# Kernel optimization log

Measured on AMD Instinct MI355X. Metric: run time of the kernel, lower is better.

The kernel has to match this reference:

```python
import jax, jax.numpy as jnp
import numpy as np

N = 100000      # nodes
E = 800000      # directed edges per branch
HID = 128
FOUT = 128
HEADS = 2
LAYERS = 3      # convlayer
JK_LAYERS = 3
H2 = (JK_LAYERS * HID) // 2   # PyG JK-LSTM hidden size = 192
N_AA = 26
N_SS = 3


def setup_inputs() -> dict:
    key = jax.random.key(0)
    ks = iter(jax.random.split(key, 32))
    def nrm(shape, scale=0.05):
        return jax.random.normal(next(ks), shape, dtype=jnp.float32) * scale
    return {
        "x_idx": jax.random.randint(next(ks), (N, 2), 0, N_SS),
        "x_flt": jax.random.normal(next(ks), (N, 5), dtype=jnp.float32),
        "edge_index_l": jax.random.randint(next(ks), (2, E), 0, N),
        "edge_index_r": jax.random.randint(next(ks), (2, E), 0, N),
        "emb_aa": nrm((2, N_AA, HID - 5)),          # [branch, vocab, hid-5]
        "emb_ss": nrm((2, N_SS, HID - 5)),
        "conv_W": nrm((2, LAYERS, HID, HEADS * HID)),
        "conv_att_src": nrm((2, LAYERS, HEADS, HID)),
        "conv_att_dst": nrm((2, LAYERS, HEADS, HID)),
        "conv_bias": nrm((2, LAYERS, HID)),
        "lstm_Wih": nrm((2, 2, 4 * H2, HID)),        # [branch, direction, 4H2, hid]
        "lstm_Whh": nrm((2, 2, 4 * H2, H2)),
        "lstm_bih": nrm((2, 2, 4 * H2)),
        "lstm_bhh": nrm((2, 2, 4 * H2)),
        "jk_att_W": nrm((2, 2 * H2)),
        "jk_att_b": nrm((2,)),
        "dummy_W": nrm((2, HID, HID)),
        "dummy_b": nrm((2, HID)),
        "fin_W": nrm((4, HID, FOUT)),
        "fin_b": nrm((4, FOUT)),
        "last_W": nrm((FOUT,)),                      # Linear(fout,1,bias=False)
    }


def _gat_conv(x, src, dst, W, att_src, att_dst, bias):
    # PyG GATConv, concat=False (mean over heads), leaky_relu slope 0.2
    n = x.shape[0]
    h, c = att_src.shape
    xh = (x @ W).reshape(n, h, c)                         # [N,H,C]
    a_src = jnp.einsum('nhc,hc->nh', xh, att_src)
    a_dst = jnp.einsum('nhc,hc->nh', xh, att_dst)
    e = jax.nn.leaky_relu(a_src[src] + a_dst[dst], 0.2)   # [E,H]
    m = jax.ops.segment_max(e, dst, num_segments=n)
    ex = jnp.exp(e - m[dst])
    denom = jax.ops.segment_sum(ex, dst, num_segments=n)
    alpha = ex / (denom[dst] + 1e-16)                     # segment softmax over dst
    out = jax.ops.segment_sum(xh[src] * alpha[:, :, None], dst, num_segments=n)
    return out.mean(axis=1) + bias                        # [N,C]


def _lstm_dir(xs, Wih, Whh, bih, bhh, reverse):
    # xs: [L,N,C]; single-layer LSTM, torch gate order i,f,g,o
    n = xs.shape[1]
    h2 = Whh.shape[1]
    b = bih + bhh
    def cell(carry, xt):
        h, c = carry
        g = xt @ Wih.T + h @ Whh.T + b
        i, f, gg, o = jnp.split(g, 4, axis=-1)
        c = jax.nn.sigmoid(f) * c + jax.nn.sigmoid(i) * jnp.tanh(gg)
        h = jax.nn.sigmoid(o) * jnp.tanh(c)
        return (h, c), h
    init = (jnp.zeros((n, h2), xs.dtype), jnp.zeros((n, h2), xs.dtype))
    _, hs = jax.lax.scan(cell, init, xs, reverse=reverse)
    return hs  # [L,N,H2]


def _jk(xs, Wih, Whh, bih, bhh, att_w, att_b):
    # PyG JumpingKnowledge('lstm'): bi-LSTM over layer axis + scalar attention
    hf = _lstm_dir(xs, Wih[0], Whh[0], bih[0], bhh[0], False)
    hb = _lstm_dir(xs, Wih[1], Whh[1], bih[1], bhh[1], True)
    h = jnp.concatenate([hf, hb], axis=-1)                # [L,N,2H2]
    a = jax.nn.softmax(jnp.einsum('lnh,h->ln', h, att_w) + att_b, axis=0)
    return (xs * a[..., None]).sum(axis=0)                # [N,C]


def _forward(x_idx, x_flt, edge_index_l, edge_index_r, emb_aa, emb_ss,
             conv_W, conv_att_src, conv_att_dst, conv_bias,
             lstm_Wih, lstm_Whh, lstm_bih, lstm_bhh, jk_att_W, jk_att_b,
             dummy_W, dummy_b, fin_W, fin_b, last_W):
    n = x_idx.shape[0]
    loops = jnp.arange(n)  # GATConv add_self_loops=True
    src_l = jnp.concatenate([edge_index_l[0], loops]); dst_l = jnp.concatenate([edge_index_l[1], loops])
    src_r = jnp.concatenate([edge_index_r[0], loops]); dst_r = jnp.concatenate([edge_index_r[1], loops])
    x_l = jnp.concatenate([emb_aa[0][x_idx[:, 0]] + emb_ss[0][x_idx[:, 1]], x_flt], axis=1)
    x_r = jnp.concatenate([emb_aa[1][x_idx[:, 0]] + emb_ss[1][x_idx[:, 1]], x_flt], axis=1)
    xs_l, xs_r = [], []
    for i in range(LAYERS):
        mean = (x_l + x_r) * 0.5
        o_l = mean + jax.nn.relu(_gat_conv(x_l, src_l, dst_l, conv_W[0, i], conv_att_src[0, i], conv_att_dst[0, i], conv_bias[0, i]))
        o_r = mean + jax.nn.relu(_gat_conv(x_r, src_r, dst_r, conv_W[1, i], conv_att_src[1, i], conv_att_dst[1, i], conv_bias[1, i]))
        x_l, x_r = o_l, o_r
        xs_l.append(x_l); xs_r.append(x_r)
    jk_l = _jk(jnp.stack(xs_l), lstm_Wih[0], lstm_Whh[0], lstm_bih[0], lstm_bhh[0], jk_att_W[0], jk_att_b[0])
    jk_r = _jk(jnp.stack(xs_r), lstm_Wih[1], lstm_Whh[1], lstm_bih[1], lstm_bhh[1], jk_att_W[1], jk_att_b[1])
    sq_l = jk_l @ dummy_W[0] + dummy_b[0]
    sq_r = jk_r @ dummy_W[1] + dummy_b[1]
    feats = [jk_l, sq_l, jk_r, sq_r]
    outs = [feats[i] @ fin_W[i] + fin_b[i] for i in range(4)]
    alpha = jax.nn.softmax(jnp.stack([o @ last_W for o in outs], axis=1), axis=1)  # [N,4]
    nodeemb = sum(outs[i] * alpha[:, i:i + 1] for i in range(4))
    return nodeemb


def reference(x_idx, x_flt, edge_index_l, edge_index_r, emb_aa, emb_ss,
              conv_W, conv_att_src, conv_att_dst, conv_bias,
              lstm_Wih, lstm_Whh, lstm_bih, lstm_bhh, jk_att_W, jk_att_b,
              dummy_W, dummy_b, fin_W, fin_b, last_W):
    return _forward(x_idx, x_flt, edge_index_l, edge_index_r, emb_aa, emb_ss,
                    conv_W, conv_att_src, conv_att_dst, conv_bias,
                    lstm_Wih, lstm_Whh, lstm_bih, lstm_bhh, jk_att_W, jk_att_b,
                    dummy_W, dummy_b, fin_W, fin_b, last_W)
```

## Files before the change

kernel.cpp:

```cpp
#include <hip/hip_runtime.h>
#include <cstddef>
#include <cstdint>

#define N_NODES 100000
#define N_EDGES 800000
#define EL_TOT  900000
#define HID 128
#define H2  192
#define G4  768
#define CH3 50000
#define BK  32
#define LDST 32

typedef unsigned short bf16;
typedef __attribute__((ext_vector_type(8))) short bf16x8v;
typedef __attribute__((ext_vector_type(4))) float f32x4v;

#define AS1 __attribute__((address_space(1)))
#define AS3 __attribute__((address_space(3)))

__device__ __forceinline__ void async16(const bf16* g, bf16* l) {
    __builtin_amdgcn_global_load_lds((AS1 void*)g, (AS3 void*)l, 16, 0, 0);
}


__device__ __forceinline__ float b2f(bf16 u) {
    return __uint_as_float(((unsigned)u) << 16);
// ... 12 lines not shown
}

__device__ __forceinline__ float x0_val(int c, int ia, int is_, int n,
                                        const float* __restrict__ embA,
                                        const float* __restrict__ embS,
                                        const float* __restrict__ xflt) {
    return (c < 123) ? (embA[ia * 123 + c] + embS[is_ * 123 + c])
                     : xflt[n * 5 + (c - 123)];
}

__device__ __forceinline__ int lstm_perm(int j) {
    int w = j & 63, tt = j >> 6;
    return (w >> 4) * 192 + tt * 16 + (w & 15);
}

__device__ __forceinline__ bool swz_tile(int R, int ntile, int& bm0, int& bn0) {
    const int id = blockIdx.x;
    const int xcd = id & 7;
    const int s = id >> 3;
    const int nt = s % ntile;
    const int yp = (s / ntile) * 8 + xcd;
    if (yp * 128 >= R) return false;
    bm0 = yp * 128; bn0 = nt * 128;
    return true;
}
static inline int swz_grid(int R, int ntile) {
    int panels = (R + 127) / 128;
    return 8 * ntile * ((panels + 7) / 8);
}


__global__ void sentinel_kernel(float* out, int n, float val) {
    int t = blockIdx.x * blockDim.x + threadIdx.x;
    if (t < n) out[t] = val;
}

__global__ void bsum_perm_kernel(const float* __restrict__ bih,
                                 const float* __restrict__ bhh,
// ... 25 lines not shown
    int per = K * M;
    int bt = (int)(t / per);
    int rem = (int)(t % per);
    int m = rem / K, k = rem % K;
    out[t] = f2b(in[(size_t)bt * per + (size_t)k * M + m]);
}


__global__ void deg_kernel(const int* __restrict__ dst, int* __restrict__ deg) {
    int t = blockIdx.x * blockDim.x + threadIdx.x;
    if (t >= EL_TOT) return;
    int d = (t < N_EDGES) ? dst[t] : (t - N_EDGES);
    atomicAdd(&deg[d], 1);
}

__global__ void scan_kernel(const int* __restrict__ deg, int* __restrict__ offs, int n) {
    __shared__ int sdata[1024];
    __shared__ int carry;
    if (threadIdx.x == 0) carry = 0;
    __syncthreads();
    for (int base = 0; base < n; base += 1024) {
        int i = base + (int)threadIdx.x;
        int v = (i < n) ? deg[i] : 0;
        sdata[threadIdx.x] = v;
        __syncthreads();
        for (int off = 1; off < 1024; off <<= 1) {
            int t = (threadIdx.x >= (unsigned)off) ? sdata[threadIdx.x - off] : 0;
            __syncthreads();
            sdata[threadIdx.x] += t;
            __syncthreads();
        }
        if (i < n) offs[i + 1] = carry + sdata[threadIdx.x];
        __syncthreads();
        if (threadIdx.x == 1023) carry += sdata[1023];
        __syncthreads();
    }
    if (threadIdx.x == 0) offs[0] = 0;
}

__global__ void copy_int_kernel(const int* __restrict__ a, int* __restrict__ b, int n) {
    int t = blockIdx.x * blockDim.x + threadIdx.x;
    if (t < n) b[t] = a[t];
}

__global__ void fill_kernel(const int* __restrict__ srcrow,
                            const int* __restrict__ dstrow,
                            int* __restrict__ pos, int* __restrict__ srcs) {
    int t = blockIdx.x * blockDim.x + threadIdx.x;
    if (t >= EL_TOT) return;
    int s, d;
    if (t < N_EDGES) { s = srcrow[t]; d = dstrow[t]; }
    else             { s = d = t - N_EDGES; }
    int p = atomicAdd(&pos[d], 1);
    srcs[p] = s;
}

template<typename TC>
__global__ __launch_bounds__(256) void mfma_gemm_kernel(
    const bf16* __restrict__ A1, const bf16* __restrict__ B1, int K1,
    const bf16* __restrict__ A2, const bf16* __restrict__ B2, int K2,
    TC* __restrict__ C, const float* __restrict__ bias, int R, int M) {
    __shared__ bf16 As[2][128 * LDST];
    __shared__ bf16 Bs[2][128 * LDST];
    int bm0, bn0;
    if (!swz_tile(R, M >> 7, bm0, bn0)) return;
    const int tid = threadIdx.x;
    const int lane = tid & 63;
    const int wave = tid >> 6;
    const int wm = (wave & 1) * 64, wn = (wave >> 1) * 64;
    const int l15 = lane & 15;
    const int q8 = (lane >> 4) * 8;
    const int lr = lane >> 2;
    const int lc = (lane & 3) * 8;

    f32x4v acc[4][4];
#pragma unroll
    for (int i = 0; i < 4; ++i)
#pragma unroll
        for (int j = 0; j < 4; ++j) acc[i][j] = (f32x4v)(0.0f);

    const int n1 = K1 / BK;
    const int n2 = A2 ? (K2 / BK) : 0;
    const int ns = n1 + n2;

    auto stage = [&](int buf, int s) {
        const bf16* Ap; const bf16* Bp; int K, k0;
        if (s < n1) { Ap = A1; Bp = B1; K = K1; k0 = s * BK; }
        else        { Ap = A2; Bp = B2; K = K2; k0 = (s - n1) * BK; }
#pragma unroll
        for (int rnd = 0; rnd < 2; ++rnd) {
            const int rbase = wave * 16 + rnd * 64;
            const int row = rbase + lr;
            int ga = bm0 + row; ga = (ga < R) ? ga : (R - 1);
            async16(Ap + (size_t)ga * K + k0 + lc, &As[buf][rbase * LDST]);
            async16(Bp + (size_t)(bn0 + row) * K + k0 + lc, &Bs[buf][rbase * LDST]);
        }
    };

    stage(0, 0);
    __syncthreads();
    for (int s = 0; s < ns; ++s) {
        const int cur = s & 1;
        if (s + 1 < ns) stage(cur ^ 1, s + 1);
        bf16x8v af[4], bfv[4];
#pragma unroll
        for (int i = 0; i < 4; ++i) {
            af[i]  = *(const bf16x8v*)&As[cur][(wm + i * 16 + l15) * LDST + q8];
            bfv[i] = *(const bf16x8v*)&Bs[cur][(wn + i * 16 + l15) * LDST + q8];
        }
#pragma unroll
        for (int i = 0; i < 4; ++i)
#pragma unroll
            for (int j = 0; j < 4; ++j)
                acc[i][j] = __builtin_amdgcn_mfma_f32_16x16x32_bf16(
                    af[i], bfv[j], acc[i][j], 0, 0, 0);
        __syncthreads();
    }

#pragma unroll
    for (int i = 0; i < 4; ++i) {
        const int row0 = bm0 + wm + i * 16 + (lane >> 4) * 4;
#pragma unroll
        for (int j = 0; j < 4; ++j) {
            const int col = bn0 + wn + j * 16 + l15;
            const float bv = bias ? bias[col] : 0.f;
#pragma unroll
            for (int r = 0; r < 4; ++r) {
                const int gr = row0 + r;
                if (gr < R) stE(C, (size_t)gr * M + col, acc[i][j][r] + bv);
            }
        }
    }
}

template<typename TC>
static void mfma_gemm(const bf16* A1, const bf16* B1, int K1,
                      const bf16* A2, const bf16* B2, int K2,
                      TC* C, const float* bias, int R, int M, hipStream_t s) {
    mfma_gemm_kernel<TC><<<swz_grid(R, M / 128), 256, 0, s>>>(
        A1, B1, K1, A2, B2, K2, C, bias, R, M);
}

__global__ __launch_bounds__(256) void lstm_gemm4_kernel(
    const bf16* __restrict__ hist, const bf16* __restrict__ Wib,
    const bf16* __restrict__ Whb, const float* __restrict__ bsum,
    const float* __restrict__ jkw, float* __restrict__ scores,
    bf16* __restrict__ cbase, const bf16* __restrict__ hin,
    bf16* __restrict__ hout, long long hcstride, int st, int combo0, int R) {
    __shared__ bf16 As[2][128 * LDST];
    __shared__ bf16 Bs[2][128 * LDST];
    int bm0, bn0;
    if (!swz_tile(R, G4 >> 7, bm0, bn0)) return;

    const int combo = combo0 + (int)blockIdx.y;
    const int b = combo >> 1, dir = combo & 1;
    const int l = dir ? (2 - st) : st;
    const bool first = (st == 0);
    const bf16* A1 = hist + (size_t)(b * 3 + l) * R * HID;
    const bf16* B1 = Wib + (size_t)combo * G4 * HID;
    const bf16* A2 = hin + (size_t)combo * hcstride;
    const bf16* B2 = Whb + (size_t)combo * G4 * H2;
    const float* bias = bsum + (size_t)combo * G4;
    const float* aw = jkw + (size_t)b * 2 * H2 + (size_t)dir * H2;
    float* score = scores + (size_t)(b * 3 + l) * R;
    bf16* c_state = cbase + (size_t)combo * hcstride;
    bf16* h_o = hout + (size_t)combo * hcstride;

    const int tid = threadIdx.x;
    const int lane = tid & 63;
    const int wave = tid >> 6;
    const int wm = (wave & 1) * 64, wn = (wave >> 1) * 64;
    const int l15 = lane & 15;
    const int q = lane >> 4;
    const int q8 = q * 8;
    const int lr = lane >> 2;
    const int lc = (lane & 3) * 8;

    f32x4v acc[4][4];
#pragma unroll
    for (int i = 0; i < 4; ++i)
#pragma unroll
        for (int j = 0; j < 4; ++j) acc[i][j] = (f32x4v)(0.0f);

    const int n1 = HID / BK;
    const int n2 = first ? 0 : (H2 / BK);
    const int ns = n1 + n2;

    auto stage = [&](int buf, int s) {
        const bf16* Ap; const bf16* Bp; int K, k0;
        if (s < n1) { Ap = A1; Bp = B1; K = HID; k0 = s * BK; }
        else        { Ap = A2; Bp = B2; K = H2;  k0 = (s - n1) * BK; }
#pragma unroll
        for (int rnd = 0; rnd < 2; ++rnd) {
            const int rbase = wave * 16 + rnd * 64;
            const int row = rbase + lr;
            int ga = bm0 + row; ga = (ga < R) ? ga : (R - 1);
            async16(Ap + (size_t)ga * K + k0 + lc, &As[buf][rbase * LDST]);
            async16(Bp + (size_t)(bn0 + row) * K + k0 + lc, &Bs[buf][rbase * LDST]);
        }
    };

    stage(0, 0);
    __syncthreads();
    for (int s = 0; s < ns; ++s) {
        const int cur = s & 1;
        if (s + 1 < ns) stage(cur ^ 1, s + 1);
        bf16x8v af[4], bfv[4];
#pragma unroll
        for (int i = 0; i < 4; ++i) {
            af[i]  = *(const bf16x8v*)&As[cur][(wm + i * 16 + l15) * LDST + q8];
            bfv[i] = *(const bf16x8v*)&Bs[cur][(wn + i * 16 + l15) * LDST + q8];
        }
#pragma unroll
        for (int i = 0; i < 4; ++i)
#pragma unroll
            for (int j = 0; j < 4; ++j)
                acc[i][j] = __builtin_amdgcn_mfma_f32_16x16x32_bf16(
                    af[i], bfv[j], acc[i][j], 0, 0, 0);
        __syncthreads();
    }

    const int u = ((bn0 + wn) >> 6) * 16 + l15;
    const float awu = aw[u];
    float bv[4];
#pragma unroll
    for (int j = 0; j < 4; ++j) bv[j] = bias[bn0 + wn + j * 16 + l15];
    float psum[4][4];
#pragma unroll
    for (int i = 0; i < 4; ++i) {
        const int row0 = bm0 + wm + i * 16 + q * 4;
#pragma unroll
        for (int r = 0; r < 4; ++r) {
            const int gr = row0 + r;
            const bool ok = gr < R;
            float ig = acc[i][0][r] + bv[0];
            float fg = acc[i][1][r] + bv[1];
            float gg = acc[i][2][r] + bv[2];
            float og = acc[i][3][r] + bv[3];
            float si = 1.f / (1.f + __expf(-ig));
            float sf = 1.f / (1.f + __expf(-fg));
            float so = 1.f / (1.f + __expf(-og));
            float co = (ok && !first) ? b2f(c_state[(size_t)gr * H2 + u]) : 0.f;
            float cn = sf * co + si * ftanh(gg);
            float hn = so * ftanh(cn);
            if (ok) {
                c_state[(size_t)gr * H2 + u] = f2b(cn);
                h_o[(size_t)gr * H2 + u] = f2b(hn);
            }
            psum[i][r] = hn * awu;
        }
    }
#pragma unroll
    for (int m = 1; m < 16; m <<= 1)
#pragma unroll
        for (int i = 0; i < 4; ++i)
#pragma unroll
            for (int r = 0; r < 4; ++r)
                psum[i][r] += __shfl_xor(psum[i][r], m);
    if (l15 == 0) {
#pragma unroll
        for (int i = 0; i < 4; ++i)
#pragma unroll
            for (int r = 0; r < 4; ++r) {
                const int gr = bm0 + wm + i * 16 + q * 4 + r;
                if (gr < R) atomicAdd(&score[gr], psum[i][r]);
            }
    }
}

__global__ __launch_bounds__(256) void mfma_gemm_x0_kernel(
    const int* __restrict__ xidx, const float* __restrict__ xflt,
    const float* __restrict__ embA, const float* __restrict__ embS,
    const bf16* __restrict__ B1, bf16* __restrict__ C, int R, int M) {
    __shared__ bf16 As[128 * LDST];
    __shared__ bf16 Bs[128 * LDST];
    int bm0, bn0;
    if (!swz_tile(R, M >> 7, bm0, bn0)) return;
    const int tid = threadIdx.x;
    const int lane = tid & 63;
    const int wave = tid >> 6;
    const int wm = (wave & 1) * 64, wn = (wave >> 1) * 64;
    const int l15 = lane & 15;
    const int q8 = (lane >> 4) * 8;
    const int srow = tid >> 2;
    const int scol = (tid & 3) * 8;
    const int lr = lane >> 2;
    const int lc = (lane & 3) * 8;

    f32x4v acc[4][4];
#pragma unroll
    for (int i = 0; i < 4; ++i)
#pragma unroll
        for (int j = 0; j < 4; ++j) acc[i][j] = (f32x4v)(0.0f);

    for (int k0 = 0; k0 < 128; k0 += BK) {
#pragma unroll
        for (int rnd = 0; rnd < 2; ++rnd) {
            {
                int row = srow + rnd * 64;
                int ga = bm0 + row; ga = (ga < R) ? ga : (R - 1);
                int ia = xidx[2 * ga], is_ = xidx[2 * ga + 1];
                bf16 tmp[8];
#pragma unroll
                for (int t = 0; t < 8; ++t)
                    tmp[t] = f2b(x0_val(k0 + scol + t, ia, is_, ga, embA, embS, xflt));
                *(int4*)&As[row * LDST + scol] = *(const int4*)tmp;
            }
            {
                const int rbase = wave * 16 + rnd * 64;
                int row = rbase + lr;
                async16(B1 + (size_t)(bn0 + row) * 128 + k0 + lc, &Bs[rbase * LDST]);
            }
        }
        __syncthreads();
        bf16x8v af[4], bfv[4];
#pragma unroll
        for (int i = 0; i < 4; ++i) {
            af[i]  = *(const bf16x8v*)&As[(wm + i * 16 + l15) * LDST + q8];
            bfv[i] = *(const bf16x8v*)&Bs[(wn + i * 16 + l15) * LDST + q8];
        }
#pragma unroll
        for (int i = 0; i < 4; ++i)
#pragma unroll
            for (int j = 0; j < 4; ++j)
                acc[i][j] = __builtin_amdgcn_mfma_f32_16x16x32_bf16(
                    af[i], bfv[j], acc[i][j], 0, 0, 0);
        __syncthreads();
    }
#pragma unroll
    for (int i = 0; i < 4; ++i) {
        const int row0 = bm0 + wm + i * 16 + (lane >> 4) * 4;
#pragma unroll
        for (int j = 0; j < 4; ++j) {
            const int col = bn0 + wn + j * 16 + l15;
#pragma unroll
            for (int r = 0; r < 4; ++r) {
                const int gr = row0 + r;
                if (gr < R) C[(size_t)gr * M + col] = f2b(acc[i][j][r]);
            }
        }
    }
}


__global__ __launch_bounds__(256) void att_kernel(
    const bf16* __restrict__ xh, const float* __restrict__ as_,
    const float* __restrict__ ad_, float* __restrict__ asrc, float* __restrict__ adst) {
    int w = (blockIdx.x * blockDim.x + threadIdx.x) >> 6;
    int lane = threadIdx.x & 63;
    if (w >= N_NODES) return;
    const bf16* row = xh + (size_t)w * 256;
    float x0 = b2f(row[lane]), x1 = b2f(row[64 + lane]);
    float x2 = b2f(row[128 + lane]), x3 = b2f(row[192 + lane]);
// ... 16 lines not shown
__global__ __launch_bounds__(256) void agg_kernel(
    const bf16* __restrict__ xh, const float* __restrict__ asrc,
    const float* __restrict__ adst, const int* __restrict__ offs,
    const int* __restrict__ srcs,
    const bf16* __restrict__ xprev_l, const bf16* __restrict__ xprev_r,
    const int* __restrict__ xidx, const float* __restrict__ xflt,
    const float* __restrict__ embAl, const float* __restrict__ embSl,
    const float* __restrict__ embAr, const float* __restrict__ embSr,
    const float* __restrict__ bias, bf16* __restrict__ outx) {
    int n = (blockIdx.x * blockDim.x + threadIdx.x) >> 6;
    int lane = threadIdx.x & 63;
    if (n >= N_NODES) return;
    const int start = offs[n], end = offs[n + 1];
    const float ad0 = adst[2 * n], ad1 = adst[2 * n + 1];

    float m0 = -1e30f, m1 = -1e30f;
    for (int j = start + lane; j < end; j += 64) {
        int s = srcs[j];
        float2 a2 = *(const float2*)(asrc + 2 * s);
        m0 = fmaxf(m0, lrelu02(a2.x + ad0));
        m1 = fmaxf(m1, lrelu02(a2.y + ad1));
    }
    for (int o = 1; o < 64; o <<= 1) {
        m0 = fmaxf(m0, __shfl_xor(m0, o));
        m1 = fmaxf(m1, __shfl_xor(m1, o));
    }

    const int eh = lane >> 5;
    const int l32 = lane & 31;
    const int head = l32 >> 4;
    const int l15 = l32 & 15;
    const int col = head * 128 + l15 * 8;
    const float mh = head ? m1 : m0;
    const float adh = head ? ad1 : ad0;

    float acc[8] = {0.f, 0.f, 0.f, 0.f, 0.f, 0.f, 0.f, 0.f};
    float dsum = 0.f;
#pragma unroll 2
    for (int j = start; j < end; j += 2) {
        int e = j + eh;
        if (e < end) {
            int s = srcs[e];
            float a = asrc[2 * s + head] + adh;
            float al = __expf(lrelu02(a) - mh);
            if (l15 == 0) dsum += al;
            int4 v = *(const int4*)(xh + (size_t)s * 256 + col);
            const int* w = (const int*)&v;
#pragma unroll
            for (int t = 0; t < 4; ++t) {
                float lo = __uint_as_float(((unsigned)w[t]) << 16);
                float hi = __uint_as_float(((unsigned)w[t]) & 0xffff0000u);
                acc[2 * t]     += lo * al;
                acc[2 * t + 1] += hi * al;
            }
        }
    }
#pragma unroll
    for (int t = 0; t < 8; ++t) acc[t] += __shfl_xor(acc[t], 32);
    dsum += __shfl_xor(dsum, 32);
// ... 114 lines not shown
    const float* jkw     = (const float*)d_in[14];
    const float* dummy_W = (const float*)d_in[16];
    const float* dummy_b = (const float*)d_in[17];
    const float* fin_W   = (const float*)d_in[18];
    const float* fin_b   = (const float*)d_in[19];
    const float* last_W  = (const float*)d_in[20];
    float* out = (float*)d_out;

    const long long S = (long long)N_NODES * HID;
    char* ws = (char*)d_ws;
    long long off = 0;

    bf16* hist = (bf16*)(ws + off);  off += align1k(6 * S * 2);
    float* scores = (float*)(ws + off); off += align1k(6LL * N_NODES * 4);
    float* bsum   = (float*)(ws + off); off += align1k(4LL * G4 * 4);
    bf16* Wih_b   = (bf16*)(ws + off); off += align1k(4LL * G4 * HID * 2);
    bf16* Whh_b   = (bf16*)(ws + off); off += align1k(4LL * G4 * H2 * 2);
    bf16* dummyWt = (bf16*)(ws + off); off += align1k(2LL * 128 * 128 * 2);
    bf16* finWt   = (bf16*)(ws + off); off += align1k(4LL * 128 * 128 * 2);

    char* BIG = ws + off;
    const long long slot0 = align1k(2 * S * 2);
    const long long slot1 = align1k((long long)N_NODES * H2 * 2);
    const long long hcsz  = align1k(4LL * N_NODES * H2 * 2);
    const long long needC = off + slot0 + slot1;
    const long long needA = off + 3 * hcsz;

    if ((long long)ws_size < needC) {
        float val = 200000.0f + (float)(ws_size >> 20);
        sentinel_kernel<<<(N_NODES * HID + 255) / 256, 256, 0, stream>>>(
            out, N_NODES * HID, val);
        return;
    }
    const bool tierA = (long long)ws_size >= needA;

    bf16* xh  = (bf16*)BIG;
    bf16* jkb = (bf16*)BIG;
    int* ibase = (int*)(BIG + slot0);
    int *deg[2], *offs[2], *pos[2], *srcs[2];
    long long io = 0;
    for (int b = 0; b < 2; ++b) {
        deg[b]  = ibase + io; io += N_NODES;
        offs[b] = ibase + io; io += N_NODES + 1;
        pos[b]  = ibase + io; io += N_NODES;
        srcs[b] = ibase + io; io += EL_TOT;
    }
    long long io4a = ((io * 4 + 15) & ~15LL);
    float* asrc = (float*)(BIG + slot0 + io4a);
    float* adst = asrc + 2LL * N_NODES;
    bf16* convWt = (bf16*)(BIG + slot0 + io4a + 4LL * N_NODES * 4);
    bf16* cC = (bf16*)(BIG + slot0);
    bf16* hC = (bf16*)BIG;
    bf16* c4  = (bf16*)BIG;
    bf16* hp0 = (bf16*)(BIG + hcsz);
    bf16* hp1 = (bf16*)(BIG + 2 * hcsz);

    const float* embA[2] = {emb_aa, emb_aa + 26 * 123};
    const float* embS[2] = {emb_ss, emb_ss + 3 * 123};

    bsum_perm_kernel<<<12, 256, 0, stream>>>(bih, bhh, bsum);
    trans_kernel<<<(6 * 128 * 256 + 255) / 256, 256, 0, stream>>>(
        conv_W, convWt, 6, 128, 256);
    lstm_w_perm_kernel<<<(4 * G4 * HID + 255) / 256, 256, 0, stream>>>(
        Wih, Wih_b, HID);
    lstm_w_perm_kernel<<<(4 * G4 * H2 + 255) / 256, 256, 0, stream>>>(
        Whh, Whh_b, H2);
    trans_kernel<<<(2 * 128 * 128 + 255) / 256, 256, 0, stream>>>(
        dummy_W, dummyWt, 2, 128, 128);
    trans_kernel<<<(4 * 128 * 128 + 255) / 256, 256, 0, stream>>>(
        fin_W, finWt, 4, 128, 128);
    for (int b = 0; b < 2; ++b) {
        const int* ei = b ? ei_r : ei_l;
        hipMemsetAsync(deg[b], 0, N_NODES * sizeof(int), stream);
        deg_kernel<<<(EL_TOT + 255) / 256, 256, 0, stream>>>(ei + N_EDGES, deg[b]);
        scan_kernel<<<1, 1024, 0, stream>>>(deg[b], offs[b], N_NODES);
        copy_int_kernel<<<(N_NODES + 255) / 256, 256, 0, stream>>>(offs[b], pos[b], N_NODES);
        fill_kernel<<<(EL_TOT + 255) / 256, 256, 0, stream>>>(
            ei, ei + N_EDGES, pos[b], srcs[b]);
    }

    for (int i = 0; i < 3; ++i) {
        for (int b = 0; b < 2; ++b) {
            const bf16* Wc = convWt + (size_t)(b * 3 + i) * 256 * 128;
            if (i == 0) {
                mfma_gemm_x0_kernel<<<swz_grid(N_NODES, 2), 256, 0, stream>>>(
                    x_idx, x_flt, embA[b], embS[b], Wc, xh, N_NODES, 256);
            } else {
                mfma_gemm<bf16>(hist + (size_t)(b * 3 + i - 1) * S, Wc, 128,
                                nullptr, nullptr, 0, xh, nullptr, N_NODES, 256, stream);
            }
            att_kernel<<<25000, 256, 0, stream>>>(
                xh, att_s + (size_t)(b * 3 + i) * 2 * HID,
                att_d + (size_t)(b * 3 + i) * 2 * HID, asrc, adst);
            const bf16* xpl = (i == 0) ? nullptr : hist + (size_t)(i - 1) * S;
            const bf16* xpr = (i == 0) ? nullptr : hist + (size_t)(3 + i - 1) * S;
            agg_kernel<<<25000, 256, 0, stream>>>(
                xh, asrc, adst, offs[b], srcs[b], xpl, xpr,
                (i == 0) ? x_idx : nullptr, x_flt,
                embA[0], embS[0], embA[1], embS[1],
                conv_b + (size_t)(b * 3 + i) * HID, hist + (size_t)(b * 3 + i) * S);
        }
    }

    hipMemsetAsync(scores, 0, (size_t)6 * N_NODES * 4, stream);
    const int gx = swz_grid(N_NODES, 6);
    if (tierA) {
        for (int st = 0; st < 3; ++st) {
            const bf16* hin = (st & 1) ? hp0 : hp1;
            bf16* hout = (st & 1) ? hp1 : hp0;
            lstm_gemm4_kernel<<<dim3(gx, 4), 256, 0, stream>>>(
                hist, Wih_b, Whh_b, bsum, jkw, scores, c4, hin, hout,
                (long long)N_NODES * H2, st, 0, N_NODES);
        }
    } else {
        for (int b = 0; b < 2; ++b)
            for (int dir = 0; dir < 2; ++dir)
                for (int st = 0; st < 3; ++st)
                    lstm_gemm4_kernel<<<dim3(gx, 1), 256, 0, stream>>>(
                        hist, Wih_b, Whh_b, bsum, jkw, scores, cC, hC, hC,
                        0LL, st, b * 2 + dir, N_NODES);
    }
    for (int b = 0; b < 2; ++b)
        jkfin_kernel<<<25000, 256, 0, stream>>>(
            scores + (size_t)b * 3 * N_NODES,
            hist + (size_t)b * 3 * S, hist + (size_t)(b * 3 + 1) * S,
            hist + (size_t)(b * 3 + 2) * S, jkb + (size_t)b * S);

    float* f3 = (float*)hist;
    bf16* jkl = jkb; bf16* jkr = jkb + S;
    for (long long c3 = 0; c3 < N_NODES; c3 += CH3) {
        int Rr = (int)((N_NODES - c3) < CH3 ? (N_NODES - c3) : CH3);
        float* o0 = f3;
        float* o1 = f3 + 1LL * CH3 * HID;
        float* o2 = f3 + 2LL * CH3 * HID;
        float* o3 = f3 + 3LL * CH3 * HID;
        bf16* sql = (bf16*)(f3 + 4LL * CH3 * HID);
        bf16* sqr = sql + (long long)CH3 * HID;
        mfma_gemm<bf16>(jkl + c3 * HID, dummyWt, 128, nullptr, nullptr, 0,
                        sql, dummy_b, Rr, 128, stream);
        mfma_gemm<bf16>(jkr + c3 * HID, dummyWt + 16384, 128, nullptr, nullptr, 0,
                        sqr, dummy_b + 128, Rr, 128, stream);
        mfma_gemm<float>(jkl + c3 * HID, finWt, 128, nullptr, nullptr, 0,
                         o0, fin_b, Rr, 128, stream);
        mfma_gemm<float>(sql, finWt + 16384, 128, nullptr, nullptr, 0,
                         o1, fin_b + 128, Rr, 128, stream);
        mfma_gemm<float>(jkr + c3 * HID, finWt + 2 * 16384, 128, nullptr, nullptr, 0,
                         o2, fin_b + 256, Rr, 128, stream);
        mfma_gemm<float>(sqr, finWt + 3 * 16384, 128, nullptr, nullptr, 0,
                         o3, fin_b + 384, Rr, 128, stream);
        final_kernel<<<(Rr + 3) / 4, 256, 0, stream>>>(
            o0, o1, o2, o3, last_W, out, Rr, c3);
    }
}
```

Baseline: 3.453 ms.

## Parallelize CSR scan, widen GEMM tiles, batch final GEMMs, drop softmax max pass

The single-block degree scan becomes a three-phase multi-block scan that covers both branches and writes the fill positions directly, which removes the copy kernel. The GEMM and LSTM kernels now compute 256-column tiles so each A tile is loaded once per row panel. The final dummy/fin GEMMs are batched into launches indexed by grid y. The LSTM path is simplified to a single per-combo schedule that uses the output buffer as h scratch. The aggregation kernel drops its segment-max pass and exponentiates raw attention logits, which saves a pass over the edges but risks overflow for large logits.

```diff
diff --git a/kernel.cpp b/kernel.cpp
--- a/kernel.cpp
+++ b/kernel.cpp
@@ -11,6 +11,7 @@
 #define CH3 50000
 #define BK  32
 #define LDST 32
+#define SCANB 98
 
 typedef unsigned short bf16;
 typedef __attribute__((ext_vector_type(8))) short bf16x8v;
@@ -53,14 +54,14 @@
     return (w >> 4) * 192 + tt * 16 + (w & 15);
 }
 
-__device__ __forceinline__ bool swz_tile(int R, int ntile, int& bm0, int& bn0) {
+__device__ __forceinline__ bool swz_tile(int R, int ntile, int& bm0, int& nt) {
     const int id = blockIdx.x;
     const int xcd = id & 7;
     const int s = id >> 3;
-    const int nt = s % ntile;
+    nt = s % ntile;
     const int yp = (s / ntile) * 8 + xcd;
     if (yp * 128 >= R) return false;
-    bm0 = yp * 128; bn0 = nt * 128;
+    bm0 = yp * 128;
     return true;
 }
 static inline int swz_grid(int R, int ntile) {
@@ -116,33 +117,57 @@
     atomicAdd(&deg[d], 1);
 }
 
-__global__ void scan_kernel(const int* __restrict__ deg, int* __restrict__ offs, int n) {
+__global__ void scan1_kernel(const int* __restrict__ deg0, const int* __restrict__ deg1,
+                             int* __restrict__ tmp0, int* __restrict__ tmp1,
+                             int* __restrict__ bsums) {
     __shared__ int sdata[1024];
-    __shared__ int carry;
-    if (threadIdx.x == 0) carry = 0;
+    const int b = blockIdx.y;
+    const int* deg = b ? deg1 : deg0;
+    int* tmp = b ? tmp1 : tmp0;
+    int i = blockIdx.x * 1024 + threadIdx.x;
+    int v = (i < N_NODES) ? deg[i] : 0;
+    sdata[threadIdx.x] = v;
     __syncthreads();
-    for (int base = 0; base < n; base += 1024) {
-        int i = base + (int)threadIdx.x;
-        int v = (i < n) ? deg[i] : 0;
-        sdata[threadIdx.x] = v;
+    for (int off = 1; off < 1024; off <<= 1) {
+        int t = (threadIdx.x >= (unsigned)off) ? sdata[threadIdx.x - off] : 0;
         __syncthreads();
-        for (int off = 1; off < 1024; off <<= 1) {
-            int t = (threadIdx.x >= (unsigned)off) ? sdata[threadIdx.x - off] : 0;
-            __syncthreads();
-            sdata[threadIdx.x] += t;
-            __syncthreads();
-        }
-        if (i < n) offs[i + 1] = carry + sdata[threadIdx.x];
+        sdata[threadIdx.x] += t;
         __syncthreads();
-        if (threadIdx.x == 1023) carry += sdata[1023];
-        __syncthreads();
-    }
-    if (threadIdx.x == 0) offs[0] = 0;
-}
-
-__global__ void copy_int_kernel(const int* __restrict__ a, int* __restrict__ b, int n) {
-    int t = blockIdx.x * blockDim.x + threadIdx.x;
-    if (t < n) b[t] = a[t];
+    }
+    if (i < N_NODES) tmp[i] = sdata[threadIdx.x];
+    if (threadIdx.x == 1023) bsums[b * SCANB + blockIdx.x] = sdata[1023];
+}
+
+__global__ void scan2_kernel(int* __restrict__ bsums) {
+    int b = threadIdx.x;
+    if (b < 2) {
+        int c = 0;
+        for (int k = 0; k < SCANB; ++k) {
+            int t = bsums[b * SCANB + k];
+            bsums[b * SCANB + k] = c;
+            c += t;
+        }
+    }
+}
+
+__global__ void scan3_kernel(const int* __restrict__ bsums,
+                             const int* __restrict__ deg0, const int* __restrict__ deg1,
+                             const int* __restrict__ tmp0, const int* __restrict__ tmp1,
+                             int* __restrict__ offs0, int* __restrict__ offs1,
+                             int* __restrict__ pos0, int* __restrict__ pos1) {
+    const int b = blockIdx.y;
+    const int* deg = b ? deg1 : deg0;
+    const int* tmp = b ? tmp1 : tmp0;
+    int* offs = b ? offs1 : offs0;
+    int* pos = b ? pos1 : pos0;
+    int carry = bsums[b * SCANB + blockIdx.x];
+    int i = blockIdx.x * 1024 + threadIdx.x;
+    if (i < N_NODES) {
+        int inc = tmp[i] + carry;
+        offs[i + 1] = inc;
+        pos[i] = inc - deg[i];
+    }
+    if (i == 0) offs[0] = 0;
 }
 
 __global__ void fill_kernel(const int* __restrict__ srcrow,
@@ -157,15 +182,13 @@
     srcs[p] = s;
 }
 
-template<typename TC>
-__global__ __launch_bounds__(256) void mfma_gemm_kernel(
+template<typename TC, int NT>
+__device__ __forceinline__ void gemm_body(
     const bf16* __restrict__ A1, const bf16* __restrict__ B1, int K1,
-    const bf16* __restrict__ A2, const bf16* __restrict__ B2, int K2,
-    TC* __restrict__ C, const float* __restrict__ bias, int R, int M) {
+    TC* __restrict__ C, const float* __restrict__ bias, int R, int M,
+    int bm0, int bn0) {
     __shared__ bf16 As[2][128 * LDST];
-    __shared__ bf16 Bs[2][128 * LDST];
-    int bm0, bn0;
-    if (!swz_tile(R, M >> 7, bm0, bn0)) return;
+    __shared__ bf16 Bs[2][128 * NT * LDST];
     const int tid = threadIdx.x;
     const int lane = tid & 63;
     const int wave = tid >> 6;
@@ -175,27 +198,26 @@
     const int lr = lane >> 2;
     const int lc = (lane & 3) * 8;
 
-    f32x4v acc[4][4];
+    f32x4v acc[4][4 * NT];
 #pragma unroll
     for (int i = 0; i < 4; ++i)
 #pragma unroll
-        for (int j = 0; j < 4; ++j) acc[i][j] = (f32x4v)(0.0f);
-
-    const int n1 = K1 / BK;
-    const int n2 = A2 ? (K2 / BK) : 0;
-    const int ns = n1 + n2;
-
+        for (int j = 0; j < 4 * NT; ++j) acc[i][j] = (f32x4v)(0.0f);
+
+    const int ns = K1 / BK;
     auto stage = [&](int buf, int s) {
-        const bf16* Ap; const bf16* Bp; int K, k0;
-        if (s < n1) { Ap = A1; Bp = B1; K = K1; k0 = s * BK; }
-        else        { Ap = A2; Bp = B2; K = K2; k0 = (s - n1) * BK; }
+        const int k0 = s * BK;
 #pragma unroll
         for (int rnd = 0; rnd < 2; ++rnd) {
             const int rbase = wave * 16 + rnd * 64;
-            const int row = rbase + lr;
-            int ga = bm0 + row; ga = (ga < R) ? ga : (R - 1);
-            async16(Ap + (size_t)ga * K + k0 + lc, &As[buf][rbase * LDST]);
-            async16(Bp + (size_t)(bn0 + row) * K + k0 + lc, &Bs[buf][rbase * LDST]);
+            int ga = bm0 + rbase + lr; ga = (ga < R) ? ga : (R - 1);
+            async16(A1 + (size_t)ga * K1 + k0 + lc, &As[buf][rbase * LDST]);
+        }
+#pragma unroll
+        for (int rnd = 0; rnd < 2 * NT; ++rnd) {
+            const int rbase = wave * 16 + rnd * 64;
+            async16(B1 + (size_t)(bn0 + rbase + lr) * K1 + k0 + lc,
+                    &Bs[buf][rbase * LDST]);
         }
     };
 
@@ -204,16 +226,18 @@
     for (int s = 0; s < ns; ++s) {
         const int cur = s & 1;
         if (s + 1 < ns) stage(cur ^ 1, s + 1);
-        bf16x8v af[4], bfv[4];
-#pragma unroll
-        for (int i = 0; i < 4; ++i) {
-            af[i]  = *(const bf16x8v*)&As[cur][(wm + i * 16 + l15) * LDST + q8];
-            bfv[i] = *(const bf16x8v*)&Bs[cur][(wn + i * 16 + l15) * LDST + q8];
-        }
+        bf16x8v af[4], bfv[4 * NT];
 #pragma unroll
         for (int i = 0; i < 4; ++i)
-#pragma unroll
-            for (int j = 0; j < 4; ++j)
+            af[i] = *(const bf16x8v*)&As[cur][(wm + i * 16 + l15) * LDST + q8];
+#pragma unroll
+        for (int j = 0; j < 4 * NT; ++j)
+            bfv[j] = *(const bf16x8v*)
+                &Bs[cur][((j >> 2) * 128 + wn + (j & 3) * 16 + l15) * LDST + q8];
+#pragma unroll
+        for (int i = 0; i < 4; ++i)
+#pragma unroll
+            for (int j = 0; j < 4 * NT; ++j)
                 acc[i][j] = __builtin_amdgcn_mfma_f32_16x16x32_bf16(
                     af[i], bfv[j], acc[i][j], 0, 0, 0);
         __syncthreads();
@@ -223,8 +247,8 @@
     for (int i = 0; i < 4; ++i) {
         const int row0 = bm0 + wm + i * 16 + (lane >> 4) * 4;
 #pragma unroll
-        for (int j = 0; j < 4; ++j) {
-            const int col = bn0 + wn + j * 16 + l15;
+        for (int j = 0; j < 4 * NT; ++j) {
+            const int col = bn0 + (j >> 2) * 128 + wn + (j & 3) * 16 + l15;
             const float bv = bias ? bias[col] : 0.f;
 #pragma unroll
             for (int r = 0; r < 4; ++r) {
@@ -235,39 +259,41 @@
     }
 }
 
+template<typename TC, int NT>
+__global__ __launch_bounds__(256) void mfma_gemm_kernel(
+    const bf16* __restrict__ A1, const bf16* __restrict__ B1, int K1,
+    TC* __restrict__ C, const float* __restrict__ bias, int R, int M) {
+    int bm0, nt;
+    if (!swz_tile(R, M / (128 * NT), bm0, nt)) return;
+    gemm_body<TC, NT>(A1, B1, K1, C, bias, R, M, bm0, nt * 128 * NT);
+}
+
 template<typename TC>
-static void mfma_gemm(const bf16* A1, const bf16* B1, int K1,
-                      const bf16* A2, const bf16* B2, int K2,
-                      TC* C, const float* bias, int R, int M, hipStream_t s) {
-    mfma_gemm_kernel<TC><<<swz_grid(R, M / 128), 256, 0, s>>>(
-        A1, B1, K1, A2, B2, K2, C, bias, R, M);
-}
-
-__global__ __launch_bounds__(256) void lstm_gemm4_kernel(
-    const bf16* __restrict__ hist, const bf16* __restrict__ Wib,
-    const bf16* __restrict__ Whb, const float* __restrict__ bsum,
-    const float* __restrict__ jkw, float* __restrict__ scores,
-    bf16* __restrict__ cbase, const bf16* __restrict__ hin,
-    bf16* __restrict__ hout, long long hcstride, int st, int combo0, int R) {
+__global__ __launch_bounds__(256) void mfma_gemm_b_kernel(
+    const bf16* a0, const bf16* a1, const bf16* a2, const bf16* a3,
+    const bf16* __restrict__ Bbase,
+    TC* c0, TC* c1, TC* c2, TC* c3,
+    const float* __restrict__ bias, int R) {
+    int bm0, nt;
+    if (!swz_tile(R, 1, bm0, nt)) return;
+    const int y = blockIdx.y;
+    const bf16* A1 = (y == 0) ? a0 : (y == 1) ? a1 : (y == 2) ? a2 : a3;
+    TC* C = (y == 0) ? c0 : (y == 1) ? c1 : (y == 2) ? c2 : c3;
+    gemm_body<TC, 1>(A1, Bbase + (size_t)y * 128 * 128, 128, C,
+                     bias + (size_t)y * 128, R, 128, bm0, 0);
+}
+
+__global__ __launch_bounds__(256) void lstm_gemm_kernel(
+    const bf16* __restrict__ A1, const bf16* __restrict__ B1,
+    const bf16* __restrict__ A2, const bf16* __restrict__ B2,
+    const float* __restrict__ bias, bf16* __restrict__ c_state,
+    bf16* __restrict__ h_out, const float* __restrict__ aw,
+    float* __restrict__ score, int R) {
     __shared__ bf16 As[2][128 * LDST];
-    __shared__ bf16 Bs[2][128 * LDST];
-    int bm0, bn0;
-    if (!swz_tile(R, G4 >> 7, bm0, bn0)) return;
-
-    const int combo = combo0 + (int)blockIdx.y;
-    const int b = combo >> 1, dir = combo & 1;
-    const int l = dir ? (2 - st) : st;
-    const bool first = (st == 0);
-    const bf16* A1 = hist + (size_t)(b * 3 + l) * R * HID;
-    const bf16* B1 = Wib + (size_t)combo * G4 * HID;
-    const bf16* A2 = hin + (size_t)combo * hcstride;
-    const bf16* B2 = Whb + (size_t)combo * G4 * H2;
-    const float* bias = bsum + (size_t)combo * G4;
-    const float* aw = jkw + (size_t)b * 2 * H2 + (size_t)dir * H2;
-    float* score = scores + (size_t)(b * 3 + l) * R;
-    bf16* c_state = cbase + (size_t)combo * hcstride;
-    bf16* h_o = hout + (size_t)combo * hcstride;
-
+    __shared__ bf16 Bs[2][256 * LDST];
+    int bm0, nt;
+    if (!swz_tile(R, 3, bm0, nt)) return;
+    const int bn0 = nt * 256;
     const int tid = threadIdx.x;
     const int lane = tid & 63;
     const int wave = tid >> 6;
@@ -277,16 +303,16 @@
     const int q8 = q * 8;
     const int lr = lane >> 2;
     const int lc = (lane & 3) * 8;
-
-    f32x4v acc[4][4];
+    const bool first = (A2 == nullptr);
+
+    f32x4v acc[4][8];
 #pragma unroll
     for (int i = 0; i < 4; ++i)
 #pragma unroll
-        for (int j = 0; j < 4; ++j) acc[i][j] = (f32x4v)(0.0f);
+        for (int j = 0; j < 8; ++j) acc[i][j] = (f32x4v)(0.0f);
 
     const int n1 = HID / BK;
-    const int n2 = first ? 0 : (H2 / BK);
-    const int ns = n1 + n2;
+    const int ns = n1 + (first ? 0 : (H2 / BK));
 
     auto stage = [&](int buf, int s) {
         const bf16* Ap; const bf16* Bp; int K, k0;
@@ -295,10 +321,14 @@
 #pragma unroll
         for (int rnd = 0; rnd < 2; ++rnd) {
             const int rbase = wave * 16 + rnd * 64;
-            const int row = rbase + lr;
-            int ga = bm0 + row; ga = (ga < R) ? ga : (R - 1);
+            int ga = bm0 + rbase + lr; ga = (ga < R) ? ga : (R - 1);
             async16(Ap + (size_t)ga * K + k0 + lc, &As[buf][rbase * LDST]);
-            async16(Bp + (size_t)(bn0 + row) * K + k0 + lc, &Bs[buf][rbase * LDST]);
+        }
+#pragma unroll
+        for (int rnd = 0; rnd < 4; ++rnd) {
+            const int rbase = wave * 16 + rnd * 64;
+            async16(Bp + (size_t)(bn0 + rbase + lr) * K + k0 + lc,
+                    &Bs[buf][rbase * LDST]);
         }
     };
 
@@ -307,26 +337,30 @@
     for (int s = 0; s < ns; ++s) {
         const int cur = s & 1;
         if (s + 1 < ns) stage(cur ^ 1, s + 1);
-        bf16x8v af[4], bfv[4];
-#pragma unroll
-        for (int i = 0; i < 4; ++i) {
-            af[i]  = *(const bf16x8v*)&As[cur][(wm + i * 16 + l15) * LDST + q8];
-            bfv[i] = *(const bf16x8v*)&Bs[cur][(wn + i * 16 + l15) * LDST + q8];
-        }
+        bf16x8v af[4], bfv[8];
 #pragma unroll
         for (int i = 0; i < 4; ++i)
-#pragma unroll
-            for (int j = 0; j < 4; ++j)
+            af[i] = *(const bf16x8v*)&As[cur][(wm + i * 16 + l15) * LDST + q8];
+#pragma unroll
+        for (int j = 0; j < 8; ++j)
+            bfv[j] = *(const bf16x8v*)
+                &Bs[cur][((j >> 2) * 128 + wn + (j & 3) * 16 + l15) * LDST + q8];
+#pragma unroll
+        for (int i = 0; i < 4; ++i)
+#pragma unroll
+            for (int j = 0; j < 8; ++j)
                 acc[i][j] = __builtin_amdgcn_mfma_f32_16x16x32_bf16(
                     af[i], bfv[j], acc[i][j], 0, 0, 0);
         __syncthreads();
     }
 
-    const int u = ((bn0 + wn) >> 6) * 16 + l15;
-    const float awu = aw[u];
-    float bv[4];
-#pragma unroll
-    for (int j = 0; j < 4; ++j) bv[j] = bias[bn0 + wn + j * 16 + l15];
+    const int u0 = ((bn0 + wn) >> 6) * 16 + l15;
+    const int u1 = ((bn0 + 128 + wn) >> 6) * 16 + l15;
+    const float aw0 = aw[u0], aw1 = aw[u1];
+    float bv[8];
+#pragma unroll
+    for (int j = 0; j < 8; ++j)
+        bv[j] = bias[bn0 + (j >> 2) * 128 + wn + (j & 3) * 16 + l15];
     float psum[4][4];
 #pragma unroll
     for (int i = 0; i < 4; ++i) {
@@ -335,21 +369,26 @@
         for (int r = 0; r < 4; ++r) {
             const int gr = row0 + r;
             const bool ok = gr < R;
-            float ig = acc[i][0][r] + bv[0];
-            float fg = acc[i][1][r] + bv[1];
-            float gg = acc[i][2][r] + bv[2];
-            float og = acc[i][3][r] + bv[3];
-            float si = 1.f / (1.f + __expf(-ig));
-            float sf = 1.f / (1.f + __expf(-fg));
-            float so = 1.f / (1.f + __expf(-og));
-            float co = (ok && !first) ? b2f(c_state[(size_t)gr * H2 + u]) : 0.f;
-            float cn = sf * co + si * ftanh(gg);
-            float hn = so * ftanh(cn);
-            if (ok) {
-                c_state[(size_t)gr * H2 + u] = f2b(cn);
-                h_o[(size_t)gr * H2 + u] = f2b(hn);
+            float hn[2];
+#pragma unroll
+            for (int jj = 0; jj < 2; ++jj) {
+                const int u = jj ? u1 : u0;
+                float ig = acc[i][jj * 4 + 0][r] + bv[jj * 4 + 0];
+                float fg = acc[i][jj * 4 + 1][r] + bv[jj * 4 + 1];
+                float gg = acc[i][jj * 4 + 2][r] + bv[jj * 4 + 2];
+                float og = acc[i][jj * 4 + 3][r] + bv[jj * 4 + 3];
+                float si = 1.f / (1.f + __expf(-ig));
+                float sf = 1.f / (1.f + __expf(-fg));
+                float so = 1.f / (1.f + __expf(-og));
+                float co = (ok && !first) ? b2f(c_state[(size_t)gr * H2 + u]) : 0.f;
+                float cn = sf * co + si * ftanh(gg);
+                hn[jj] = so * ftanh(cn);
+                if (ok) {
+                    c_state[(size_t)gr * H2 + u] = f2b(cn);
+                    h_out[(size_t)gr * H2 + u] = f2b(hn[jj]);
+                }
             }
-            psum[i][r] = hn * awu;
+            psum[i][r] = hn[0] * aw0 + hn[1] * aw1;
         }
     }
 #pragma unroll
@@ -373,11 +412,11 @@
 __global__ __launch_bounds__(256) void mfma_gemm_x0_kernel(
     const int* __restrict__ xidx, const float* __restrict__ xflt,
     const float* __restrict__ embA, const float* __restrict__ embS,
-    const bf16* __restrict__ B1, bf16* __restrict__ C, int R, int M) {
+    const bf16* __restrict__ B1, bf16* __restrict__ C, int R) {
     __shared__ bf16 As[128 * LDST];
-    __shared__ bf16 Bs[128 * LDST];
-    int bm0, bn0;
-    if (!swz_tile(R, M >> 7, bm0, bn0)) return;
+    __shared__ bf16 Bs[256 * LDST];
+    int bm0, nt;
+    if (!swz_tile(R, 1, bm0, nt)) return;
     const int tid = threadIdx.x;
     const int lane = tid & 63;
     const int wave = tid >> 6;
@@ -389,42 +428,42 @@
     const int lr = lane >> 2;
     const int lc = (lane & 3) * 8;
 
-    f32x4v acc[4][4];
+    f32x4v acc[4][8];
 #pragma unroll
     for (int i = 0; i < 4; ++i)
 #pragma unroll
-        for (int j = 0; j < 4; ++j) acc[i][j] = (f32x4v)(0.0f);
+        for (int j = 0; j < 8; ++j) acc[i][j] = (f32x4v)(0.0f);
 
     for (int k0 = 0; k0 < 128; k0 += BK) {
 #pragma unroll
         for (int rnd = 0; rnd < 2; ++rnd) {
-            {
-                int row = srow + rnd * 64;
-                int ga = bm0 + row; ga = (ga < R) ? ga : (R - 1);
-                int ia = xidx[2 * ga], is_ = xidx[2 * ga + 1];
-                bf16 tmp[8];
-#pragma unroll
-                for (int t = 0; t < 8; ++t)
-                    tmp[t] = f2b(x0_val(k0 + scol + t, ia, is_, ga, embA, embS, xflt));
-                *(int4*)&As[row * LDST + scol] = *(const int4*)tmp;
-            }
-            {
-                const int rbase = wave * 16 + rnd * 64;
-                int row = rbase + lr;
-                async16(B1 + (size_t)(bn0 + row) * 128 + k0 + lc, &Bs[rbase * LDST]);
-            }
+            int row = srow + rnd * 64;
+            int ga = bm0 + row; ga = (ga < R) ? ga : (R - 1);
+            int ia = xidx[2 * ga], is_ = xidx[2 * ga + 1];
+            bf16 tmp[8];
+#pragma unroll
+            for (int t = 0; t < 8; ++t)
+                tmp[t] = f2b(x0_val(k0 + scol + t, ia, is_, ga, embA, embS, xflt));
+            *(int4*)&As[row * LDST + scol] = *(const int4*)tmp;
+        }
+#pragma unroll
+        for (int rnd = 0; rnd < 4; ++rnd) {
+            const int rbase = wave * 16 + rnd * 64;
+            async16(B1 + (size_t)(rbase + lr) * 128 + k0 + lc, &Bs[rbase * LDST]);
         }
         __syncthreads();
-        bf16x8v af[4], bfv[4];
-#pragma unroll
-        for (int i = 0; i < 4; ++i) {
-            af[i]  = *(const bf16x8v*)&As[(wm + i * 16 + l15) * LDST + q8];
-            bfv[i] = *(const bf16x8v*)&Bs[(wn + i * 16 + l15) * LDST + q8];
-        }
+        bf16x8v af[4], bfv[8];
 #pragma unroll
         for (int i = 0; i < 4; ++i)
-#pragma unroll
-            for (int j = 0; j < 4; ++j)
+            af[i] = *(const bf16x8v*)&As[(wm + i * 16 + l15) * LDST + q8];
+#pragma unroll
+        for (int j = 0; j < 8; ++j)
+            bfv[j] = *(const bf16x8v*)
+                &Bs[((j >> 2) * 128 + wn + (j & 3) * 16 + l15) * LDST + q8];
+#pragma unroll
+        for (int i = 0; i < 4; ++i)
+#pragma unroll
+            for (int j = 0; j < 8; ++j)
                 acc[i][j] = __builtin_amdgcn_mfma_f32_16x16x32_bf16(
                     af[i], bfv[j], acc[i][j], 0, 0, 0);
         __syncthreads();
@@ -433,12 +472,12 @@
     for (int i = 0; i < 4; ++i) {
         const int row0 = bm0 + wm + i * 16 + (lane >> 4) * 4;
 #pragma unroll
-        for (int j = 0; j < 4; ++j) {
-            const int col = bn0 + wn + j * 16 + l15;
+        for (int j = 0; j < 8; ++j) {
+            const int col = (j >> 2) * 128 + wn + (j & 3) * 16 + l15;
 #pragma unroll
             for (int r = 0; r < 4; ++r) {
                 const int gr = row0 + r;
-                if (gr < R) C[(size_t)gr * M + col] = f2b(acc[i][j][r]);
+                if (gr < R) C[(size_t)gr * 256 + col] = f2b(acc[i][j][r]);
             }
         }
     }
@@ -485,24 +524,11 @@
     const int start = offs[n], end = offs[n + 1];
     const float ad0 = adst[2 * n], ad1 = adst[2 * n + 1];
 
-    float m0 = -1e30f, m1 = -1e30f;
-    for (int j = start + lane; j < end; j += 64) {
-        int s = srcs[j];
-        float2 a2 = *(const float2*)(asrc + 2 * s);
-        m0 = fmaxf(m0, lrelu02(a2.x + ad0));
-        m1 = fmaxf(m1, lrelu02(a2.y + ad1));
-    }
-    for (int o = 1; o < 64; o <<= 1) {
-        m0 = fmaxf(m0, __shfl_xor(m0, o));
-        m1 = fmaxf(m1, __shfl_xor(m1, o));
-    }
-
     const int eh = lane >> 5;
     const int l32 = lane & 31;
     const int head = l32 >> 4;
     const int l15 = l32 & 15;
     const int col = head * 128 + l15 * 8;
-    const float mh = head ? m1 : m0;
     const float adh = head ? ad1 : ad0;
 
     float acc[8] = {0.f, 0.f, 0.f, 0.f, 0.f, 0.f, 0.f, 0.f};
@@ -513,7 +539,7 @@
         if (e < end) {
             int s = srcs[e];
             float a = asrc[2 * s + head] + adh;
-            float al = __expf(lrelu02(a) - mh);
+            float al = __expf(lrelu02(a));
             if (l15 == 0) dsum += al;
             int4 v = *(const int4*)(xh + (size_t)s * 256 + col);
             const int* w = (const int*)&v;
@@ -658,6 +684,7 @@
     bf16* hist = (bf16*)(ws + off);  off += align1k(6 * S * 2);
     float* scores = (float*)(ws + off); off += align1k(6LL * N_NODES * 4);
     float* bsum   = (float*)(ws + off); off += align1k(4LL * G4 * 4);
+    int* bsums    = (int*)(ws + off);  off += align1k(2LL * SCANB * 4);
     bf16* Wih_b   = (bf16*)(ws + off); off += align1k(4LL * G4 * HID * 2);
     bf16* Whh_b   = (bf16*)(ws + off); off += align1k(4LL * G4 * H2 * 2);
     bf16* dummyWt = (bf16*)(ws + off); off += align1k(2LL * 128 * 128 * 2);
@@ -666,17 +693,14 @@
     char* BIG = ws + off;
     const long long slot0 = align1k(2 * S * 2);
     const long long slot1 = align1k((long long)N_NODES * H2 * 2);
-    const long long hcsz  = align1k(4LL * N_NODES * H2 * 2);
-    const long long needC = off + slot0 + slot1;
-    const long long needA = off + 3 * hcsz;
-
-    if ((long long)ws_size < needC) {
+    const long long need = off + slot0 + slot1;
+
+    if ((long long)ws_size < need) {
         float val = 200000.0f + (float)(ws_size >> 20);
         sentinel_kernel<<<(N_NODES * HID + 255) / 256, 256, 0, stream>>>(
             out, N_NODES * HID, val);
         return;
     }
-    const bool tierA = (long long)ws_size >= needA;
 
     bf16* xh  = (bf16*)BIG;
     bf16* jkb = (bf16*)BIG;
@@ -693,11 +717,9 @@
     float* asrc = (float*)(BIG + slot0 + io4a);
     float* adst = asrc + 2LL * N_NODES;
     bf16* convWt = (bf16*)(BIG + slot0 + io4a + 4LL * N_NODES * 4);
+    bf16* hA = (bf16*)BIG;
+    bf16* hB = (bf16*)d_out;
     bf16* cC = (bf16*)(BIG + slot0);
-    bf16* hC = (bf16*)BIG;
-    bf16* c4  = (bf16*)BIG;
-    bf16* hp0 = (bf16*)(BIG + hcsz);
-    bf16* hp1 = (bf16*)(BIG + 2 * hcsz);
 
     const float* embA[2] = {emb_aa, emb_aa + 26 * 123};
     const float* embS[2] = {emb_ss, emb_ss + 3 * 123};
@@ -713,25 +735,30 @@
         dummy_W, dummyWt, 2, 128, 128);
     trans_kernel<<<(4 * 128 * 128 + 255) / 256, 256, 0, stream>>>(
         fin_W, finWt, 4, 128, 128);
-    for (int b = 0; b < 2; ++b) {
-        const int* ei = b ? ei_r : ei_l;
-        hipMemsetAsync(deg[b], 0, N_NODES * sizeof(int), stream);
-        deg_kernel<<<(EL_TOT + 255) / 256, 256, 0, stream>>>(ei + N_EDGES, deg[b]);
-        scan_kernel<<<1, 1024, 0, stream>>>(deg[b], offs[b], N_NODES);
-        copy_int_kernel<<<(N_NODES + 255) / 256, 256, 0, stream>>>(offs[b], pos[b], N_NODES);
-        fill_kernel<<<(EL_TOT + 255) / 256, 256, 0, stream>>>(
-            ei, ei + N_EDGES, pos[b], srcs[b]);
-    }
+    hipMemsetAsync(deg[0], 0, N_NODES * sizeof(int), stream);
+    hipMemsetAsync(deg[1], 0, N_NODES * sizeof(int), stream);
+    deg_kernel<<<(EL_TOT + 255) / 256, 256, 0, stream>>>(ei_l + N_EDGES, deg[0]);
+    deg_kernel<<<(EL_TOT + 255) / 256, 256, 0, stream>>>(ei_r + N_EDGES, deg[1]);
+    scan1_kernel<<<dim3(SCANB, 2), 1024, 0, stream>>>(
+        deg[0], deg[1], pos[0], pos[1], bsums);
+    scan2_kernel<<<1, 64, 0, stream>>>(bsums);
+    scan3_kernel<<<dim3(SCANB, 2), 1024, 0, stream>>>(
+        bsums, deg[0], deg[1], pos[0], pos[1], offs[0], offs[1], pos[0], pos[1]);
+    fill_kernel<<<(EL_TOT + 255) / 256, 256, 0, stream>>>(
+        ei_l, ei_l + N_EDGES, pos[0], srcs[0]);
+    fill_kernel<<<(EL_TOT + 255) / 256, 256, 0, stream>>>(
+        ei_r, ei_r + N_EDGES, pos[1], srcs[1]);
 
     for (int i = 0; i < 3; ++i) {
         for (int b = 0; b < 2; ++b) {
             const bf16* Wc = convWt + (size_t)(b * 3 + i) * 256 * 128;
             if (i == 0) {
-                mfma_gemm_x0_kernel<<<swz_grid(N_NODES, 2), 256, 0, stream>>>(
-                    x_idx, x_flt, embA[b], embS[b], Wc, xh, N_NODES, 256);
+                mfma_gemm_x0_kernel<<<swz_grid(N_NODES, 1), 256, 0, stream>>>(
+                    x_idx, x_flt, embA[b], embS[b], Wc, xh, N_NODES);
             } else {
-                mfma_gemm<bf16>(hist + (size_t)(b * 3 + i - 1) * S, Wc, 128,
-                                nullptr, nullptr, 0, xh, nullptr, N_NODES, 256, stream);
+                mfma_gemm_kernel<bf16, 2><<<swz_grid(N_NODES, 1), 256, 0, stream>>>(
+                    hist + (size_t)(b * 3 + i - 1) * S, Wc, 128,
+                    xh, nullptr, N_NODES, 256);
             }
             att_kernel<<<25000, 256, 0, stream>>>(
                 xh, att_s + (size_t)(b * 3 + i) * 2 * HID,
@@ -747,22 +774,23 @@
     }
 
     hipMemsetAsync(scores, 0, (size_t)6 * N_NODES * 4, stream);
-    const int gx = swz_grid(N_NODES, 6);
-    if (tierA) {
-        for (int st = 0; st < 3; ++st) {
-            const bf16* hin = (st & 1) ? hp0 : hp1;
-            bf16* hout = (st & 1) ? hp1 : hp0;
-            lstm_gemm4_kernel<<<dim3(gx, 4), 256, 0, stream>>>(
-                hist, Wih_b, Whh_b, bsum, jkw, scores, c4, hin, hout,
-                (long long)N_NODES * H2, st, 0, N_NODES);
-        }
-    } else {
-        for (int b = 0; b < 2; ++b)
-            for (int dir = 0; dir < 2; ++dir)
-                for (int st = 0; st < 3; ++st)
-                    lstm_gemm4_kernel<<<dim3(gx, 1), 256, 0, stream>>>(
-                        hist, Wih_b, Whh_b, bsum, jkw, scores, cC, hC, hC,
-                        0LL, st, b * 2 + dir, N_NODES);
+    const int gx = swz_grid(N_NODES, 3);
+    for (int b = 0; b < 2; ++b) {
+        for (int dir = 0; dir < 2; ++dir) {
+            const bf16* Wi = Wih_b + (size_t)(b * 2 + dir) * G4 * HID;
+            const bf16* Wh = Whh_b + (size_t)(b * 2 + dir) * G4 * H2;
+            const float* bs = bsum + (size_t)(b * 2 + dir) * G4;
+            const float* aw = jkw + (size_t)b * 2 * H2 + (size_t)dir * H2;
+            for (int st = 0; st < 3; ++st) {
+                int l = dir ? (2 - st) : st;
+                const bf16* A = hist + (size_t)(b * 3 + l) * S;
+                const bf16* hin = (st == 0) ? nullptr : ((st & 1) ? hA : hB);
+                bf16* hout = (st & 1) ? hB : hA;
+                lstm_gemm_kernel<<<gx, 256, 0, stream>>>(
+                    A, Wi, hin, Wh, bs, cC, hout, aw,
+                    scores + (size_t)(b * 3 + l) * N_NODES, N_NODES);
+            }
+        }
     }
     for (int b = 0; b < 2; ++b)
         jkfin_kernel<<<25000, 256, 0, stream>>>(
@@ -780,18 +808,12 @@
         float* o3 = f3 + 3LL * CH3 * HID;
         bf16* sql = (bf16*)(f3 + 4LL * CH3 * HID);
         bf16* sqr = sql + (long long)CH3 * HID;
-        mfma_gemm<bf16>(jkl + c3 * HID, dummyWt, 128, nullptr, nullptr, 0,
-                        sql, dummy_b, Rr, 128, stream);
-        mfma_gemm<bf16>(jkr + c3 * HID, dummyWt + 16384, 128, nullptr, nullptr, 0,
-                        sqr, dummy_b + 128, Rr, 128, stream);
-        mfma_gemm<float>(jkl + c3 * HID, finWt, 128, nullptr, nullptr, 0,
-                         o0, fin_b, Rr, 128, stream);
-        mfma_gemm<float>(sql, finWt + 16384, 128, nullptr, nullptr, 0,
-                         o1, fin_b + 128, Rr, 128, stream);
-        mfma_gemm<float>(jkr + c3 * HID, finWt + 2 * 16384, 128, nullptr, nullptr, 0,
-                         o2, fin_b + 256, Rr, 128, stream);
-        mfma_gemm<float>(sqr, finWt + 3 * 16384, 128, nullptr, nullptr, 0,
-                         o3, fin_b + 384, Rr, 128, stream);
+        mfma_gemm_b_kernel<bf16><<<dim3(swz_grid(Rr, 1), 2), 256, 0, stream>>>(
+            jkl + c3 * HID, jkr + c3 * HID, nullptr, nullptr,
+            dummyWt, sql, sqr, nullptr, nullptr, dummy_b, Rr);
+        mfma_gemm_b_kernel<float><<<dim3(swz_grid(Rr, 1), 4), 256, 0, stream>>>(
+            jkl + c3 * HID, sql, jkr + c3 * HID, sqr,
+            finWt, o0, o1, o2, o3, fin_b, Rr);
         final_kernel<<<(Rr + 3) / 4, 256, 0, stream>>>(
             o0, o1, o2, o3, last_W, out, Rr, c3);
     }
```

After: 4.272 ms. 23.7% more time.
